# Kernel tuning notes

Hardware: AMD Instinct MI355X
Metric: run time of the kernel (lower is better)

Reference implementation:

```python
import jax, jax.numpy as jnp
import numpy as np

N_NODES = 50000
N_EDGES = 800000
IN_F = 128
HID = 128
OUT = 2


def setup_inputs() -> dict:
    key = jax.random.key(0)
    ks = jax.random.split(key, 10)
    x = jax.random.normal(ks[0], (N_NODES, IN_F), dtype=jnp.float32)
    edge_index = jax.random.randint(ks[1], (2, N_EDGES), 0, N_NODES, dtype=jnp.int64)

    def lin(k, fan_in, fan_out):
        s = 1.0 / np.sqrt(fan_in)
        return jax.random.uniform(k, (fan_in, fan_out), jnp.float32, -s, s)

    return {
        "x": x,
        "edge_index": edge_index,
        # SAGEConv1: lin_l applied to mean-aggregated neighbors (with bias),
        # lin_r applied to root features (no bias), PyG convention.
        "W1_l": lin(ks[2], IN_F, HID),
        "W1_r": lin(ks[3], IN_F, HID),
        "b1": jnp.zeros((HID,), jnp.float32),
        "W2_l": lin(ks[4], HID, HID),
        "W2_r": lin(ks[5], HID, HID),
        "b2": jnp.zeros((HID,), jnp.float32),
        "Wfc": lin(ks[6], HID, OUT),
        "bfc": jnp.zeros((OUT,), jnp.float32),
    }


def reference(x, edge_index, W1_l, W1_r, b1, W2_l, W2_r, b2, Wfc, bfc):
    n = x.shape[0]
    src = edge_index[0]  # message source j
    dst = edge_index[1]  # aggregation target i
    # in-degree for mean aggregation (clamp to avoid div-by-zero for isolated nodes)
    deg = jax.ops.segment_sum(jnp.ones_like(dst, dtype=x.dtype), dst, num_segments=n)
    inv_deg = 1.0 / jnp.maximum(deg, 1.0)  # [n]

    def sage_conv(h, Wl, Wr, b):
        # mean over incoming neighbor features, then two linear maps
        agg = jax.ops.segment_sum(h[src], dst, num_segments=n) * inv_deg[:, None]
        return agg @ Wl + h @ Wr + b

    # dropout is identity at inference (training=False)
    h = jax.nn.relu(sage_conv(x, W1_l, W1_r, b1))
    h = jax.nn.relu(sage_conv(h, W2_l, W2_r, b2))
    return h @ Wfc + bfc  # [n, out] logits
```

## Files before the change

### kernel.cpp

```cpp
#include <hip/hip_runtime.h>

#define NN 50000
#define NE 800000
#define BSHIFT 9
#define NB_BUCKET ((NN + 511) >> BSHIFT)
#define BCAP 16384
#define EPB 2048
#define NBLK_E ((NE + EPB - 1) / EPB)

#define CVT_BLKS 6250
#define PREP_BLKS 32
#define SETUP_GRID (CVT_BLKS + PREP_BLKS + 1)

typedef short short8 __attribute__((ext_vector_type(8)));
typedef short short4v __attribute__((ext_vector_type(4)));
typedef float f32x4 __attribute__((ext_vector_type(4)));
typedef _Float16 half8v __attribute__((ext_vector_type(8)));

__device__ inline unsigned short f16_bits(float f) {
    _Float16 h = (_Float16)f;
    return __builtin_bit_cast(unsigned short, h);
}

__global__ __launch_bounds__(256) void setup_kernel(const float* __restrict__ x,
                                                    unsigned short* __restrict__ xb,
                                                    const float* __restrict__ W0,
                                                    const float* __restrict__ W1,
                                                    const float* __restrict__ W2,
                                                    const float* __restrict__ W3,
                                                    short* __restrict__ wf,
                                                    int* __restrict__ cursor0) {
    int b = blockIdx.x;
    if (b < CVT_BLKS) {
        int i = b * 256 + threadIdx.x;
        float4 v = ((const float4*)x)[i];
        short4v r;
        r[0] = (short)f16_bits(v.x);
        r[1] = (short)f16_bits(v.y);
        r[2] = (short)f16_bits(v.z);
        r[3] = (short)f16_bits(v.w);
        ((short4v*)xb)[i] = r;
    } else if (b < CVT_BLKS + PREP_BLKS) {
        int t = (b - CVT_BLKS) * 256 + threadIdx.x;
        int mat = t >> 11;
        const float* W = (mat == 0) ? W0 : (mat == 1) ? W1 : (mat == 2) ? W2 : W3;
        short* out = wf + (size_t)mat * 16384;
        int r = t & 2047;
        int nt = r >> 8;
        int kc = (r >> 6) & 3;
        int lane = r & 63;
        int n = nt * 16 + (lane & 15);
        int kbase = kc * 32 + ((lane >> 4) << 3);
        short8 vh;
#pragma unroll
        for (int j = 0; j < 8; ++j) {
            float w = W[(size_t)(kbase + j) * 128 + n];
            vh[j] = (short)f16_bits(w);
        }
        size_t o = ((size_t)((nt * 4 + kc) * 64 + lane)) * 8;
        *(short8*)(out + o) = vh;
    } else {
        if (threadIdx.x < NB_BUCKET) cursor0[threadIdx.x] = 0;
    }
}

__global__ __launch_bounds__(256) void binA_kernel(const int* __restrict__ src,
                                                   const int* __restrict__ dst,
                                                   int* __restrict__ cursor0,
                                                   unsigned* __restrict__ packed, int ne) {
    __shared__ int cnt[NB_BUCKET];
    __shared__ int gstart[NB_BUCKET];
    __shared__ int cur[NB_BUCKET];
    int t = threadIdx.x;
    if (t < NB_BUCKET) cnt[t] = 0;
    __syncthreads();
    int base = blockIdx.x * EPB + t * 8;
    int s[8], d[8];
    int m = 0;
    if (base + 8 <= ne) {
        *(int4*)&s[0] = *(const int4*)(src + base);
        *(int4*)&s[4] = *(const int4*)(src + base + 4);
        *(int4*)&d[0] = *(const int4*)(dst + base);
        *(int4*)&d[4] = *(const int4*)(dst + base + 4);
        m = 8;
    } else if (base < ne) {
        m = ne - base;
        for (int i = 0; i < m; ++i) { s[i] = src[base + i]; d[i] = dst[base + i]; }
    }
    for (int i = 0; i < m; ++i) atomicAdd(&cnt[d[i] >> BSHIFT], 1);
    __syncthreads();
    if (t < NB_BUCKET) {
        gstart[t] = t * BCAP + atomicAdd(&cursor0[t], cnt[t]);
        cur[t] = 0;
    }
    __syncthreads();
    for (int i = 0; i < m; ++i) {
        int b = d[i] >> BSHIFT;
        int l = atomicAdd(&cur[b], 1);
        packed[gstart[b] + l] = ((unsigned)(d[i] & 511) << 16) | (unsigned)s[i];
    }
}

__global__ __launch_bounds__(512) void binB_kernel(const unsigned* __restrict__ packed,
                                                   const int* __restrict__ cursor0,
                                                   int* __restrict__ row_ptr,
                                                   float* __restrict__ inv_deg,
                                                   int* __restrict__ col, int n, int ne) {
    __shared__ int sdeg[512];
    __shared__ int scur[512];
    __shared__ int scnt[NB_BUCKET];
    __shared__ int sebeg[NB_BUCKET];
    int b = blockIdx.x, t = threadIdx.x;
    if (t < NB_BUCKET) scnt[t] = cursor0[t];
    sdeg[t] = 0;
    __syncthreads();
    if (t == 0) {
        int run = 0;
        for (int i = 0; i < NB_BUCKET; ++i) { sebeg[i] = run; run += scnt[i]; }
    }
    __syncthreads();
    int ebeg = sebeg[b];
    int cntE = scnt[b];
    const unsigned* pk = packed + (size_t)b * BCAP;
    for (int e = t; e < cntE; e += 512) atomicAdd(&sdeg[pk[e] >> 16], 1);
    __syncthreads();
    int v = sdeg[t];
    for (int d = 1; d < 512; d <<= 1) {
        int u = (t >= d) ? sdeg[t - d] : 0;
        __syncthreads();
        sdeg[t] += u;
        __syncthreads();
    }
    int excl = sdeg[t] - v;
    scur[t] = excl;
    int node = (b << BSHIFT) + t;
    if (node < n) {
        row_ptr[node] = ebeg + excl;
        inv_deg[node] = 1.0f / (float)(v > 0 ? v : 1);
    }
    if (b == 0 && t == 0) row_ptr[n] = ne;
    __syncthreads();
    for (int e = t; e < cntE; e += 512) {
        unsigned w = pk[e];
        int dl = w >> 16;
        int pos = ebeg + atomicAdd(&scur[dl], 1);
        col[pos] = (int)(w & 0xffffu);
    }
}

__global__ __launch_bounds__(256) void agg_kernel(const unsigned short* __restrict__ hb,
                                                  const int* __restrict__ row_ptr,
                                                  const int* __restrict__ col,
                                                  const float* __restrict__ inv_deg,
                                                  unsigned short* __restrict__ outb, int n) {
    int node = blockIdx.x * 4 + (threadIdx.x >> 6);
    if (node >= n) return;
    int lane = threadIdx.x & 63;
    int slot = lane >> 4, sub = lane & 15;
    int beg = row_ptr[node], end = row_ptr[node + 1];
    const unsigned short* base = hb + (sub << 3);
    float acc[8];
#pragma unroll
    for (int j = 0; j < 8; ++j) acc[j] = 0.f;

    int e = beg + slot;
    for (; e + 4 < end; e += 8) {
        int j0 = col[e];
        int j1 = col[e + 4];
        half8v v0 = *(const half8v*)(base + ((size_t)j0 << 7));
        half8v v1 = *(const half8v*)(base + ((size_t)j1 << 7));
#pragma unroll
        for (int j = 0; j < 8; ++j) {
            acc[j] += (float)v0[j];
            acc[j] += (float)v1[j];
        }
    }
    if (e < end) {
        int j0 = col[e];
        half8v v0 = *(const half8v*)(base + ((size_t)j0 << 7));
#pragma unroll
        for (int j = 0; j < 8; ++j) acc[j] += (float)v0[j];
    }
#pragma unroll
    for (int j = 0; j < 8; ++j) {
        acc[j] += __shfl_xor(acc[j], 16, 64);
        acc[j] += __shfl_xor(acc[j], 32, 64);
    }
    if (slot == 0) {
        float s = inv_deg[node];
        short8 o;
#pragma unroll
        for (int j = 0; j < 8; ++j) o[j] = (short)f16_bits(acc[j] * s);
        *(short8*)(outb + ((size_t)node << 7) + (sub << 3)) = o;
    }
}

__global__ __launch_bounds__(256) void gemm_mfma(const unsigned short* __restrict__ A0b,
                                                 const unsigned short* __restrict__ A1b,
                                                 const short* __restrict__ Wf0,
                                                 const short* __restrict__ Wf1,
                                                 const float* __restrict__ bias,
                                                 unsigned short* __restrict__ outb,
                                                 const float* __restrict__ Wfc,
                                                 const float* __restrict__ bfc,
                                                 float* __restrict__ fcout,
                                                 int n, int relu) {
    int lane = threadIdx.x & 63;
    int wave = threadIdx.x >> 6;
    int quad = lane >> 4, m16 = lane & 15;
    int row_base = blockIdx.x * 64 + wave * 16;
    int arow = row_base + m16;
    if (arow > n - 1) arow = n - 1;

    const unsigned short* ap0 = A0b + ((size_t)arow << 7) + (quad << 3);
    const unsigned short* ap1 = A1b + ((size_t)arow << 7) + (quad << 3);
    half8v a0[4], a1[4];
#pragma unroll
    for (int kc = 0; kc < 4; ++kc) {
        a0[kc] = *(const half8v*)(ap0 + kc * 32);
        a1[kc] = *(const half8v*)(ap1 + kc * 32);
    }

    f32x4 acc[8];
#pragma unroll
    for (int nt = 0; nt < 8; ++nt) acc[nt] = (f32x4){0.f, 0.f, 0.f, 0.f};

#pragma unroll
    for (int kc = 0; kc < 4; ++kc) {
        const short* wp0 = Wf0 + ((size_t)kc * 64 + lane) * 8;
        const short* wp1 = Wf1 + ((size_t)kc * 64 + lane) * 8;
#pragma unroll
        for (int nt = 0; nt < 8; ++nt) {
            half8v b0 = *(const half8v*)(wp0 + (size_t)nt * 2048);
            half8v b1 = *(const half8v*)(wp1 + (size_t)nt * 2048);
            acc[nt] = __builtin_amdgcn_mfma_f32_16x16x32_f16(a0[kc], b0, acc[nt], 0, 0, 0);
            acc[nt] = __builtin_amdgcn_mfma_f32_16x16x32_f16(a1[kc], b1, acc[nt], 0, 0, 0);
        }
    }

    float bcol[8];
#pragma unroll
    for (int nt = 0; nt < 8; ++nt) bcol[nt] = bias[nt * 16 + m16];

    if (Wfc) {
        float w0[8], w1[8];
#pragma unroll
        for (int nt = 0; nt < 8; ++nt) {
            float2 wv = *(const float2*)(Wfc + 2 * (nt * 16 + m16));
            w0[nt] = wv.x;
            w1[nt] = wv.y;
        }
        float b0 = bfc[0], b1 = bfc[1];
#pragma unroll
        for (int r = 0; r < 4; ++r) {
            float p0 = 0.f, p1 = 0.f;
#pragma unroll
            for (int nt = 0; nt < 8; ++nt) {
                float v = fmaxf(acc[nt][r] + bcol[nt], 0.f);
                p0 += v * w0[nt];
                p1 += v * w1[nt];
            }
#pragma unroll
            for (int off = 1; off < 16; off <<= 1) {
                p0 += __shfl_xor(p0, off, 64);
                p1 += __shfl_xor(p1, off, 64);
            }
            int row = row_base + quad * 4 + r;
            if (m16 == 0 && row < n) {
                float2 o;
                o.x = p0 + b0;
                o.y = p1 + b1;
                *(float2*)(fcout + 2 * (size_t)row) = o;
            }
        }
    } else {
#pragma unroll
        for (int r = 0; r < 4; ++r) {
            int row = row_base + quad * 4 + r;
            if (row >= n) continue;
            unsigned short* opb = outb + ((size_t)row << 7) + m16;
#pragma unroll
            for (int nt = 0; nt < 8; ++nt) {
                float v = acc[nt][r] + bcol[nt];
                if (relu) v = fmaxf(v, 0.f);
                opb[nt * 16] = f16_bits(v);
            }
        }
    }
}

extern "C" void kernel_launch(void* const* d_in, const int* in_sizes, int n_in,
                              void* d_out, int out_size, void* d_ws, size_t ws_size,
                              hipStream_t stream) {
    const float* x   = (const float*)d_in[0];
    const int* edge  = (const int*)d_in[1];
    const float* W1l = (const float*)d_in[2];
    const float* W1r = (const float*)d_in[3];
    const float* b1  = (const float*)d_in[4];
    const float* W2l = (const float*)d_in[5];
    const float* W2r = (const float*)d_in[6];
    const float* b2  = (const float*)d_in[7];
    const float* Wfc = (const float*)d_in[8];
    const float* bfc = (const float*)d_in[9];
    float* out = (float*)d_out;

    const int n = NN, ne = NE;
    const int* src = edge;
    const int* dst = edge + ne;

    char* ws = (char*)d_ws;
    size_t off = 0;
    auto alloc = [&](size_t bytes) -> char* {
        char* p = ws + off;
        off = (off + bytes + 511) & ~(size_t)511;
        return p;
    };
    int* row_ptr     = (int*)alloc((size_t)(n + 1) * 4);
    float* invdeg    = (float*)alloc((size_t)n * 4);
    int* cursor0     = (int*)alloc((size_t)NB_BUCKET * 4);
    short* wf        = (short*)alloc((size_t)4 * 16384 * 2);
    unsigned* packed = (unsigned*)alloc((size_t)NB_BUCKET * BCAP * 4);
    int* col         = (int*)alloc((size_t)ne * 4);
    unsigned short* aggb = (unsigned short*)alloc((size_t)n * 128 * 2);
    unsigned short* xb   = (unsigned short*)alloc((size_t)n * 128 * 2);
    unsigned short* h1b  = (unsigned short*)alloc((size_t)n * 128 * 2);
    (void)ws_size; (void)in_sizes; (void)n_in; (void)out_size;

    setup_kernel<<<SETUP_GRID, 256, 0, stream>>>(x, xb, W1l, W1r, W2l, W2r, wf, cursor0);
    binA_kernel<<<NBLK_E, 256, 0, stream>>>(src, dst, cursor0, packed, ne);
    binB_kernel<<<NB_BUCKET, 512, 0, stream>>>(packed, cursor0, row_ptr, invdeg, col, n, ne);

    agg_kernel<<<(n + 3) / 4, 256, 0, stream>>>(xb, row_ptr, col, invdeg, aggb, n);
    gemm_mfma<<<(n + 63) / 64, 256, 0, stream>>>(aggb, xb, wf, wf + 16384, b1, h1b,
                                                 (const float*)0, (const float*)0, (float*)0, n, 1);
    agg_kernel<<<(n + 3) / 4, 256, 0, stream>>>(h1b, row_ptr, col, invdeg, aggb, n);
    gemm_mfma<<<(n + 63) / 64, 256, 0, stream>>>(aggb, h1b, wf + 2 * 16384, wf + 3 * 16384, b2,
                                                 (unsigned short*)0, Wfc, bfc, out, n, 1);
}
```

Before: 225.1 us.

## Store features in 32-column chunk-major layout and pin feature chunks to XCDs

Feature matrices (xb, h1b, aggb) are stored chunk-major, four 32-wide fp16 column chunks of NN rows each. Aggregation is rewritten so that blockIdx mod 8 maps each chunk to a pair of XCDs, which keeps each XCD's gather working set (about 3.2 MB per chunk) small enough to stay in its L2. Each wave now handles two nodes with 16 edge slots of 4 lanes each and uses nontemporal loads and stores for the index streams and the output. The GEMM's A loads and output stores are adjusted to the new layout, which makes its output stores less contiguous. The code also relies on round-robin block-to-XCD dispatch and on NN being divisible by 16.

```diff
diff --git a/kernel.cpp b/kernel.cpp
--- a/kernel.cpp
+++ b/kernel.cpp
@@ -11,6 +11,9 @@
 #define CVT_BLKS 6250
 #define PREP_BLKS 32
 #define SETUP_GRID (CVT_BLKS + PREP_BLKS + 1)
+
+#define N16 (NN >> 4)
+#define AGGC_GRID ((((N16) + 1) / 2) * 8)
 
 typedef short short8 __attribute__((ext_vector_type(8)));
 typedef short short4v __attribute__((ext_vector_type(4)));
@@ -39,7 +42,11 @@
         r[1] = (short)f16_bits(v.y);
         r[2] = (short)f16_bits(v.z);
         r[3] = (short)f16_bits(v.w);
-        ((short4v*)xb)[i] = r;
+        int row = i >> 5;
+        int f4 = i & 31;
+        int chunk = f4 >> 3;
+        int w4 = f4 & 7;
+        ((short4v*)xb)[((size_t)chunk * NN + row) * 8 + w4] = r;
     } else if (b < CVT_BLKS + PREP_BLKS) {
         int t = (b - CVT_BLKS) * 256 + threadIdx.x;
         int mat = t >> 11;
@@ -148,50 +155,49 @@
     }
 }
 
-__global__ __launch_bounds__(256) void agg_kernel(const unsigned short* __restrict__ hb,
-                                                  const int* __restrict__ row_ptr,
-                                                  const int* __restrict__ col,
-                                                  const float* __restrict__ inv_deg,
-                                                  unsigned short* __restrict__ outb, int n) {
-    int node = blockIdx.x * 4 + (threadIdx.x >> 6);
-    if (node >= n) return;
+__global__ __launch_bounds__(512) void aggc_kernel(const unsigned short* __restrict__ hb,
+                                                   const int* __restrict__ row_ptr,
+                                                   const int* __restrict__ col,
+                                                   const float* __restrict__ inv_deg,
+                                                   unsigned short* __restrict__ outb) {
+    int xcd = blockIdx.x & 7;
+    int grp = blockIdx.x >> 3;
+    int chunk = xcd >> 1, sub = xcd & 1;
+    int node16 = grp * 2 + sub;
+    if (node16 >= N16) return;
     int lane = threadIdx.x & 63;
-    int slot = lane >> 4, sub = lane & 15;
-    int beg = row_ptr[node], end = row_ptr[node + 1];
-    const unsigned short* base = hb + (sub << 3);
-    float acc[8];
-#pragma unroll
-    for (int j = 0; j < 8; ++j) acc[j] = 0.f;
-
-    int e = beg + slot;
-    for (; e + 4 < end; e += 8) {
-        int j0 = col[e];
-        int j1 = col[e + 4];
-        half8v v0 = *(const half8v*)(base + ((size_t)j0 << 7));
-        half8v v1 = *(const half8v*)(base + ((size_t)j1 << 7));
+    int wave = threadIdx.x >> 6;
+    int slot = lane >> 2, s4 = lane & 3;
+    const unsigned short* tab = hb + (size_t)chunk * NN * 32;
+    unsigned short* outp = outb + (size_t)chunk * NN * 32;
+#pragma unroll
+    for (int i = 0; i < 2; ++i) {
+        int node = node16 * 16 + wave * 2 + i;
+        int beg = __builtin_nontemporal_load(row_ptr + node);
+        int end = __builtin_nontemporal_load(row_ptr + node + 1);
+        float acc[8];
+#pragma unroll
+        for (int j = 0; j < 8; ++j) acc[j] = 0.f;
+        for (int e = beg + slot; e < end; e += 16) {
+            int j0 = __builtin_nontemporal_load(col + e);
+            half8v v = *(const half8v*)(tab + (size_t)j0 * 32 + (s4 << 3));
+#pragma unroll
+            for (int j = 0; j < 8; ++j) acc[j] += (float)v[j];
+        }
 #pragma unroll
         for (int j = 0; j < 8; ++j) {
-            acc[j] += (float)v0[j];
-            acc[j] += (float)v1[j];
-        }
-    }
-    if (e < end) {
-        int j0 = col[e];
-        half8v v0 = *(const half8v*)(base + ((size_t)j0 << 7));
-#pragma unroll
-        for (int j = 0; j < 8; ++j) acc[j] += (float)v0[j];
-    }
-#pragma unroll
-    for (int j = 0; j < 8; ++j) {
-        acc[j] += __shfl_xor(acc[j], 16, 64);
-        acc[j] += __shfl_xor(acc[j], 32, 64);
-    }
-    if (slot == 0) {
-        float s = inv_deg[node];
-        short8 o;
-#pragma unroll
-        for (int j = 0; j < 8; ++j) o[j] = (short)f16_bits(acc[j] * s);
-        *(short8*)(outb + ((size_t)node << 7) + (sub << 3)) = o;
+            acc[j] += __shfl_xor(acc[j], 4, 64);
+            acc[j] += __shfl_xor(acc[j], 8, 64);
+            acc[j] += __shfl_xor(acc[j], 16, 64);
+            acc[j] += __shfl_xor(acc[j], 32, 64);
+        }
+        if (slot == 0) {
+            float s = inv_deg[node];
+            short8 o;
+#pragma unroll
+            for (int j = 0; j < 8; ++j) o[j] = (short)f16_bits(acc[j] * s);
+            __builtin_nontemporal_store(o, (short8*)(outp + (size_t)node * 32 + (s4 << 3)));
+        }
     }
 }
 
@@ -212,13 +218,11 @@
     int arow = row_base + m16;
     if (arow > n - 1) arow = n - 1;
 
-    const unsigned short* ap0 = A0b + ((size_t)arow << 7) + (quad << 3);
-    const unsigned short* ap1 = A1b + ((size_t)arow << 7) + (quad << 3);
     half8v a0[4], a1[4];
 #pragma unroll
     for (int kc = 0; kc < 4; ++kc) {
-        a0[kc] = *(const half8v*)(ap0 + kc * 32);
-        a1[kc] = *(const half8v*)(ap1 + kc * 32);
+        a0[kc] = *(const half8v*)(A0b + ((size_t)kc * NN + arow) * 32 + (quad << 3));
+        a1[kc] = *(const half8v*)(A1b + ((size_t)kc * NN + arow) * 32 + (quad << 3));
     }
 
     f32x4 acc[8];
@@ -278,12 +282,11 @@
         for (int r = 0; r < 4; ++r) {
             int row = row_base + quad * 4 + r;
             if (row >= n) continue;
-            unsigned short* opb = outb + ((size_t)row << 7) + m16;
 #pragma unroll
             for (int nt = 0; nt < 8; ++nt) {
                 float v = acc[nt][r] + bcol[nt];
                 if (relu) v = fmaxf(v, 0.f);
-                opb[nt * 16] = f16_bits(v);
+                outb[((size_t)(nt >> 1) * NN + row) * 32 + (nt & 1) * 16 + m16] = f16_bits(v);
             }
         }
     }
@@ -330,10 +333,10 @@
     binA_kernel<<<NBLK_E, 256, 0, stream>>>(src, dst, cursor0, packed, ne);
     binB_kernel<<<NB_BUCKET, 512, 0, stream>>>(packed, cursor0, row_ptr, invdeg, col, n, ne);
 
-    agg_kernel<<<(n + 3) / 4, 256, 0, stream>>>(xb, row_ptr, col, invdeg, aggb, n);
+    aggc_kernel<<<AGGC_GRID, 512, 0, stream>>>(xb, row_ptr, col, invdeg, aggb);
     gemm_mfma<<<(n + 63) / 64, 256, 0, stream>>>(aggb, xb, wf, wf + 16384, b1, h1b,
                                                  (const float*)0, (const float*)0, (float*)0, n, 1);
-    agg_kernel<<<(n + 3) / 4, 256, 0, stream>>>(h1b, row_ptr, col, invdeg, aggb, n);
+    aggc_kernel<<<AGGC_GRID, 512, 0, stream>>>(h1b, row_ptr, col, invdeg, aggb);
     gemm_mfma<<<(n + 63) / 64, 256, 0, stream>>>(aggb, h1b, wf + 2 * 16384, wf + 3 * 16384, b2,
                                                  (unsigned short*)0, Wfc, bfc, out, n, 1);
 }
```

Result: slower. 325.9 us (+44.8%).

## Fuse neighbor mean aggregation into MFMA GEMM kernel

Applied to the files above, without the earlier changes.

Replaces the separate aggregation and GEMM kernels with one kernel where each MFMA lane gathers and averages neighbor rows for its tile row directly into registers before the matrix multiply. This removes the intermediate aggregated buffer's write and re-read and two kernel launches per forward pass. The trade-off is far fewer waves for the gather phase (one row per 4 lanes instead of a whole wave per node), which reduces memory-level parallelism and exposes degree imbalance within a wave.

```diff
diff --git a/kernel.cpp b/kernel.cpp
--- a/kernel.cpp
+++ b/kernel.cpp
@@ -148,63 +148,18 @@
     }
 }
 
-__global__ __launch_bounds__(256) void agg_kernel(const unsigned short* __restrict__ hb,
+__global__ __launch_bounds__(256) void fused_sage(const unsigned short* __restrict__ hb,
                                                   const int* __restrict__ row_ptr,
                                                   const int* __restrict__ col,
                                                   const float* __restrict__ inv_deg,
-                                                  unsigned short* __restrict__ outb, int n) {
-    int node = blockIdx.x * 4 + (threadIdx.x >> 6);
-    if (node >= n) return;
-    int lane = threadIdx.x & 63;
-    int slot = lane >> 4, sub = lane & 15;
-    int beg = row_ptr[node], end = row_ptr[node + 1];
-    const unsigned short* base = hb + (sub << 3);
-    float acc[8];
-#pragma unroll
-    for (int j = 0; j < 8; ++j) acc[j] = 0.f;
-
-    int e = beg + slot;
-    for (; e + 4 < end; e += 8) {
-        int j0 = col[e];
-        int j1 = col[e + 4];
-        half8v v0 = *(const half8v*)(base + ((size_t)j0 << 7));
-        half8v v1 = *(const half8v*)(base + ((size_t)j1 << 7));
-#pragma unroll
-        for (int j = 0; j < 8; ++j) {
-            acc[j] += (float)v0[j];
-            acc[j] += (float)v1[j];
-        }
-    }
-    if (e < end) {
-        int j0 = col[e];
-        half8v v0 = *(const half8v*)(base + ((size_t)j0 << 7));
-#pragma unroll
-        for (int j = 0; j < 8; ++j) acc[j] += (float)v0[j];
-    }
-#pragma unroll
-    for (int j = 0; j < 8; ++j) {
-        acc[j] += __shfl_xor(acc[j], 16, 64);
-        acc[j] += __shfl_xor(acc[j], 32, 64);
-    }
-    if (slot == 0) {
-        float s = inv_deg[node];
-        short8 o;
-#pragma unroll
-        for (int j = 0; j < 8; ++j) o[j] = (short)f16_bits(acc[j] * s);
-        *(short8*)(outb + ((size_t)node << 7) + (sub << 3)) = o;
-    }
-}
-
-__global__ __launch_bounds__(256) void gemm_mfma(const unsigned short* __restrict__ A0b,
-                                                 const unsigned short* __restrict__ A1b,
-                                                 const short* __restrict__ Wf0,
-                                                 const short* __restrict__ Wf1,
-                                                 const float* __restrict__ bias,
-                                                 unsigned short* __restrict__ outb,
-                                                 const float* __restrict__ Wfc,
-                                                 const float* __restrict__ bfc,
-                                                 float* __restrict__ fcout,
-                                                 int n, int relu) {
+                                                  const short* __restrict__ Wf0,
+                                                  const short* __restrict__ Wf1,
+                                                  const float* __restrict__ bias,
+                                                  unsigned short* __restrict__ outb,
+                                                  const float* __restrict__ Wfc,
+                                                  const float* __restrict__ bfc,
+                                                  float* __restrict__ fcout,
+                                                  int n, int relu) {
     int lane = threadIdx.x & 63;
     int wave = threadIdx.x >> 6;
     int quad = lane >> 4, m16 = lane & 15;
@@ -212,14 +167,53 @@
     int arow = row_base + m16;
     if (arow > n - 1) arow = n - 1;
 
-    const unsigned short* ap0 = A0b + ((size_t)arow << 7) + (quad << 3);
-    const unsigned short* ap1 = A1b + ((size_t)arow << 7) + (quad << 3);
-    half8v a0[4], a1[4];
-#pragma unroll
-    for (int kc = 0; kc < 4; ++kc) {
-        a0[kc] = *(const half8v*)(ap0 + kc * 32);
-        a1[kc] = *(const half8v*)(ap1 + kc * 32);
-    }
+    int beg = row_ptr[arow], end = row_ptr[arow + 1];
+    float accg[4][8];
+#pragma unroll
+    for (int kc = 0; kc < 4; ++kc)
+#pragma unroll
+        for (int j = 0; j < 8; ++j) accg[kc][j] = 0.f;
+
+    const unsigned short* tq = hb + (quad << 3);
+    int e = beg;
+    for (; e + 4 <= end; e += 4) {
+        int c0 = col[e], c1 = col[e + 1], c2 = col[e + 2], c3 = col[e + 3];
+        const unsigned short* r0 = tq + ((size_t)c0 << 7);
+        const unsigned short* r1 = tq + ((size_t)c1 << 7);
+        const unsigned short* r2 = tq + ((size_t)c2 << 7);
+        const unsigned short* r3 = tq + ((size_t)c3 << 7);
+#pragma unroll
+        for (int kc = 0; kc < 4; ++kc) {
+            half8v v0 = *(const half8v*)(r0 + kc * 32);
+            half8v v1 = *(const half8v*)(r1 + kc * 32);
+            half8v v2 = *(const half8v*)(r2 + kc * 32);
+            half8v v3 = *(const half8v*)(r3 + kc * 32);
+#pragma unroll
+            for (int j = 0; j < 8; ++j)
+                accg[kc][j] += (float)v0[j] + (float)v1[j] + ((float)v2[j] + (float)v3[j]);
+        }
+    }
+    for (; e < end; ++e) {
+        const unsigned short* r0 = tq + ((size_t)col[e] << 7);
+#pragma unroll
+        for (int kc = 0; kc < 4; ++kc) {
+            half8v v0 = *(const half8v*)(r0 + kc * 32);
+#pragma unroll
+            for (int j = 0; j < 8; ++j) accg[kc][j] += (float)v0[j];
+        }
+    }
+
+    float sdeg = inv_deg[arow];
+    half8v a0[4];
+#pragma unroll
+    for (int kc = 0; kc < 4; ++kc)
+#pragma unroll
+        for (int j = 0; j < 8; ++j) a0[kc][j] = (_Float16)(accg[kc][j] * sdeg);
+
+    half8v a1[4];
+#pragma unroll
+    for (int kc = 0; kc < 4; ++kc)
+        a1[kc] = *(const half8v*)(hb + ((size_t)arow << 7) + kc * 32 + (quad << 3));
 
     f32x4 acc[8];
 #pragma unroll
@@ -321,7 +315,6 @@
     short* wf        = (short*)alloc((size_t)4 * 16384 * 2);
     unsigned* packed = (unsigned*)alloc((size_t)NB_BUCKET * BCAP * 4);
     int* col         = (int*)alloc((size_t)ne * 4);
-    unsigned short* aggb = (unsigned short*)alloc((size_t)n * 128 * 2);
     unsigned short* xb   = (unsigned short*)alloc((size_t)n * 128 * 2);
     unsigned short* h1b  = (unsigned short*)alloc((size_t)n * 128 * 2);
     (void)ws_size; (void)in_sizes; (void)n_in; (void)out_size;
@@ -330,10 +323,10 @@
     binA_kernel<<<NBLK_E, 256, 0, stream>>>(src, dst, cursor0, packed, ne);
     binB_kernel<<<NB_BUCKET, 512, 0, stream>>>(packed, cursor0, row_ptr, invdeg, col, n, ne);
 
-    agg_kernel<<<(n + 3) / 4, 256, 0, stream>>>(xb, row_ptr, col, invdeg, aggb, n);
-    gemm_mfma<<<(n + 63) / 64, 256, 0, stream>>>(aggb, xb, wf, wf + 16384, b1, h1b,
-                                                 (const float*)0, (const float*)0, (float*)0, n, 1);
-    agg_kernel<<<(n + 3) / 4, 256, 0, stream>>>(h1b, row_ptr, col, invdeg, aggb, n);
-    gemm_mfma<<<(n + 63) / 64, 256, 0, stream>>>(aggb, h1b, wf + 2 * 16384, wf + 3 * 16384, b2,
-                                                 (unsigned short*)0, Wfc, bfc, out, n, 1);
-}
+    fused_sage<<<(n + 63) / 64, 256, 0, stream>>>(xb, row_ptr, col, invdeg,
+                                                  wf, wf + 16384, b1, h1b,
+                                                  (const float*)0, (const float*)0, (float*)0, n, 1);
+    fused_sage<<<(n + 63) / 64, 256, 0, stream>>>(h1b, row_ptr, col, invdeg,
+                                                  wf + 2 * 16384, wf + 3 * 16384, b2,
+                                                  (unsigned short*)0, Wfc, bfc, out, n, 1);
+}
```

After: 230.5 us. +2.4%, slower.
